# Optimization experiments

Hardware: AMD Instinct MI355X
Metric: run time of the kernel (lower is better)

The kernel has to match this reference:

```python
import jax, jax.numpy as jnp
import numpy as np

N_FILTERS = 100
WINDOWS = (2, 3, 4, 5)
B, S, W, D = 64, 400, 16, 64
VOCAB, HID = 96, 128


def setup_inputs() -> dict:
    key = jax.random.key(0)
    ks = jax.random.split(key, 16)
    inp = {
        'char_idxs': jax.random.randint(ks[0], (B, S, W), 0, VOCAB),
        'char_vectors': jax.random.normal(ks[1], (VOCAB, D), jnp.float32),
        'filt2': jax.random.normal(ks[2], (N_FILTERS, 2 * D), jnp.float32) * 0.05,
        'filt3': jax.random.normal(ks[3], (N_FILTERS, 3 * D), jnp.float32) * 0.05,
        'filt4': jax.random.normal(ks[4], (N_FILTERS, 4 * D), jnp.float32) * 0.05,
        'filt5': jax.random.normal(ks[5], (N_FILTERS, 5 * D), jnp.float32) * 0.05,
        'w_proj': jax.random.normal(ks[6], (HID, 4 * N_FILTERS), jnp.float32) * 0.05,
        't_w0': jax.random.normal(ks[7], (HID, HID), jnp.float32) * 0.05,
        't_b0': jax.random.normal(ks[8], (HID,), jnp.float32) * 0.05,
        't_w1': jax.random.normal(ks[9], (HID, HID), jnp.float32) * 0.05,
        't_b1': jax.random.normal(ks[10], (HID,), jnp.float32) * 0.05,
        'g_w0': jax.random.normal(ks[11], (HID, HID), jnp.float32) * 0.05,
        'g_b0': jax.random.normal(ks[12], (HID,), jnp.float32) * 0.05,
        'g_w1': jax.random.normal(ks[13], (HID, HID), jnp.float32) * 0.05,
        'g_b1': jax.random.normal(ks[14], (HID,), jnp.float32) * 0.05,
    }
    return inp


def _conv_branch(embed, filt, w):
    # embed: [B, S, W, D]; filt: [100, w*D]
    b, s, wl, d = embed.shape
    L = wl - w + 1  # valid positions
    idx = jnp.arange(L)[:, None] + jnp.arange(w)  # [L, w]
    xw = embed[:, :, idx, :].reshape(b, s, L, w * d)  # [B,S,L,w*D]
    h = jnp.tanh(jnp.einsum('bslk,fk->bslf', xw, filt))  # [B,S,L,100]
    return h.max(axis=2)  # max-pool over all positions -> [B,S,100]


def reference(char_idxs, char_vectors, filt2, filt3, filt4, filt5, w_proj,
              t_w0, t_b0, t_w1, t_b1, g_w0, g_b0, g_w1, g_b1):
    embed = char_vectors[char_idxs]  # [B,S,W,D]
    outs = jnp.concatenate(
        [_conv_branch(embed, f, w) for f, w in zip((filt2, filt3, filt4, filt5), WINDOWS)],
        axis=-1)  # [B,S,400]
    x = outs @ w_proj.T  # no-bias linear -> [B,S,HID]
    # 2-layer highway: x = g*relu(Wt x + bt) + (1-g)*x, g = sigmoid(Wg x + bg)
    for tw, tb, gw, gb in ((t_w0, t_b0, g_w0, g_b0), (t_w1, t_b1, g_w1, g_b1)):
        g = jax.nn.sigmoid(x @ gw.T + gb)
        t = jax.nn.relu(x @ tw.T + tb)
        x = g * t + (1.0 - g) * x
    return x
```

## Files before the change

### kernel.cpp

```cpp
#include <hip/hip_runtime.h>

#define NT     25600
#define WCH    16
#define DIM    64
#define VOCAB  96
#define HID    128
#define FPAD   104
#define NSLOT  14
#define TROW   (NSLOT * FPAD)
#define KP     416
#define TOKB   16
#define CLP    424
#define XLP    136

typedef __attribute__((ext_vector_type(8))) _Float16 h8;
typedef __attribute__((ext_vector_type(4))) float f32x4;

__device__ __forceinline__ h8 hmax8(h8 a, h8 b) {
  h8 r;
#pragma unroll
  for (int i = 0; i < 8; ++i) r[i] = a[i] > b[i] ? a[i] : b[i];
  return r;
}

__device__ __forceinline__ float tanh_fast(float m) {
  m = fminf(fmaxf(m, -15.f), 15.f);
  float e = __expf(2.f * m);
  return (e - 1.f) / (e + 1.f);
}

__global__ __launch_bounds__(256) void k_prep(
    const float* __restrict__ cv,
    const float* __restrict__ f2, const float* __restrict__ f3,
    const float* __restrict__ f4, const float* __restrict__ f5,
    const float* __restrict__ wproj,
    const float* __restrict__ tw0, const float* __restrict__ gw0,
    const float* __restrict__ tw1, const float* __restrict__ gw1,
    _Float16* __restrict__ T, _Float16* __restrict__ wprojP,
    _Float16* __restrict__ hw) {
  __shared__ float fS[100 * 65];
  __shared__ float cvS[32 * 65];
  const int tid = threadIdx.x;
  const int b = blockIdx.x;

  if (b < 42) {
    const int slot = b / 3, cg = b % 3;
    int wi, j;
    if (slot < 2)      { wi = 0; j = slot; }
    else if (slot < 5) { wi = 1; j = slot - 2; }
    else if (slot < 9) { wi = 2; j = slot - 5; }
    else               { wi = 3; j = slot - 9; }
    const float* filt = (wi == 0) ? f2 : (wi == 1) ? f3 : (wi == 2) ? f4 : f5;
    const int rowlen = (wi + 2) * DIM;
    for (int idx = tid; idx < 100 * DIM; idx += 256) {
      int f = idx >> 6, d = idx & 63;
      fS[f * 65 + d] = filt[f * rowlen + j * DIM + d];
    }
    for (int idx = tid; idx < 32 * DIM; idx += 256) {
      int c = idx >> 6, d = idx & 63;
      cvS[c * 65 + d] = cv[(cg * 32 + c) * DIM + d];
    }
    __syncthreads();
    for (int o = tid; o < 32 * FPAD; o += 256) {
      int cl = o & 31, fo = o >> 5;
      float s = 0.f;
      if (fo < 100) {
#pragma unroll 8
        for (int d = 0; d < DIM; ++d) s += cvS[cl * 65 + d] * fS[fo * 65 + d];
      }
      T[(size_t)(cg * 32 + cl) * TROW + slot * FPAD + fo] = (_Float16)s;
    }
  } else if (b < 106) {
    const int bb = b - 42;
    const int n = bb * 2 + (tid >> 7);
    const int k0 = tid & 127;
    for (int k = k0; k < KP; k += 128) {
      int wi = (k < 104) ? 0 : (k < 208) ? 1 : (k < 312) ? 2 : 3;
      int f = k - wi * FPAD;
      wprojP[n * KP + k] =
          (f < 100) ? (_Float16)wproj[n * 400 + wi * 100 + f] : (_Float16)0.f;
    }
  } else {
    const int idx = (b - 106) * 256 + tid;
    const int which = idx >> 14, r = idx & 16383;
    const float* src = (which == 0) ? tw0 : (which == 1) ? gw0
                     : (which == 2) ? tw1 : gw1;
    hw[idx] = (_Float16)src[r];
  }
}

template<int WI>
__device__ __forceinline__ void conv_win(const _Float16* __restrict__ T,
                                         const int* __restrict__ chS,
                                         _Float16* __restrict__ convL, int tid) {
  if (tid >= TOKB * 13) return;
  constexpr int W = WI + 2, L = 15 - WI;
  constexpr int SB = (WI == 0) ? 0 : (WI == 1) ? 2 : (WI == 2) ? 5 : 9;
  const int token = (tid * 1262) >> 14;
  const int octet = tid - token * 13;
  const int* chp = chS + token * WCH;
  const _Float16* Tb = T + SB * FPAD + octet * 8;
  h8 m;
  {
    h8 s = *(const h8*)(Tb + chp[0]);
#pragma unroll
    for (int j = 1; j < W; ++j) s += *(const h8*)(Tb + chp[j] + j * FPAD);
    m = s;
  }
#pragma unroll
  for (int l = 1; l < L; ++l) {
    h8 s = *(const h8*)(Tb + chp[l]);
#pragma unroll
    for (int j = 1; j < W; ++j) s += *(const h8*)(Tb + chp[l + j] + j * FPAD);
    m = hmax8(m, s);
  }
  h8 r;
#pragma unroll
  for (int i = 0; i < 8; ++i) r[i] = (_Float16)tanh_fast((float)m[i]);
  *(h8*)(convL + token * CLP + WI * FPAD + octet * 8) = r;
}

__global__ __launch_bounds__(256) void k_fused(
    const int* __restrict__ chars,
    const _Float16* __restrict__ T,
    const _Float16* __restrict__ wprojP,
    const _Float16* __restrict__ hw,
    const float* __restrict__ tb0, const float* __restrict__ tb1,
    const float* __restrict__ gb0, const float* __restrict__ gb1,
    float* __restrict__ out) {
  __shared__ __align__(16) _Float16 convL[TOKB * CLP];
  __shared__ __align__(16) _Float16 xbf[TOKB * XLP];
  __shared__ __align__(16) int chS[TOKB * WCH];

  const int tid = threadIdx.x;
  const int wave = tid >> 6, lane = tid & 63;
  const int m16 = lane & 15, quad = lane >> 4;
  const int tok0 = blockIdx.x * TOKB;
  const f32x4 zero = {0.f, 0.f, 0.f, 0.f};

  chS[tid] = chars[tok0 * WCH + tid] * TROW;
  __syncthreads();

  conv_win<0>(T, chS, convL, tid);
  conv_win<1>(T, chS, convL, tid);
  conv_win<2>(T, chS, convL, tid);
  conv_win<3>(T, chS, convL, tid);
  __syncthreads();

  const int hcA = wave * 16 + m16;
  const int hcB = hcA + 64;
  f32x4 xpA = zero, xpB = zero;
  for (int kstep = 0; kstep < 13; ++kstep) {
    const int ko = kstep * 32 + quad * 8;
    h8 a  = *(const h8*)(convL + m16 * CLP + ko);
    h8 b0 = *(const h8*)(wprojP + (size_t)hcA * KP + ko);
    h8 b1 = *(const h8*)(wprojP + (size_t)hcB * KP + ko);
    xpA = __builtin_amdgcn_mfma_f32_16x16x32_f16(a, b0, xpA, 0, 0, 0);
    xpB = __builtin_amdgcn_mfma_f32_16x16x32_f16(a, b1, xpB, 0, 0, 0);
  }

#pragma unroll
  for (int r = 0; r < 4; ++r) {
    xbf[(quad * 4 + r) * XLP + hcA]      = (_Float16)xpA[r];
    xbf[(quad * 4 + r) * XLP + 64 + hcA] = (_Float16)xpB[r];
  }
  __syncthreads();

#pragma unroll
  for (int layer = 0; layer < 2; ++layer) {
    const _Float16* tw = hw + (layer ? 2 : 0) * HID * HID;
    const _Float16* gw = hw + (layer ? 3 : 1) * HID * HID;
    const float* tbv = layer ? tb1 : tb0;
    const float* gbv = layer ? gb1 : gb0;
    float btA = tbv[hcA], bgA = gbv[hcA];
    float btB = tbv[hcB], bgB = gbv[hcB];

    f32x4 atA = zero, atB = zero, agA = zero, agB = zero;
#pragma unroll
    for (int kstep = 0; kstep < 4; ++kstep) {
      const int ko = kstep * 32 + quad * 8;
      h8 a   = *(const h8*)(xbf + m16 * XLP + ko);
      h8 bt0 = *(const h8*)(tw + (size_t)hcA * HID + ko);
      h8 bt1 = *(const h8*)(tw + (size_t)hcB * HID + ko);
      h8 bg0 = *(const h8*)(gw + (size_t)hcA * HID + ko);
      h8 bg1 = *(const h8*)(gw + (size_t)hcB * HID + ko);
      atA = __builtin_amdgcn_mfma_f32_16x16x32_f16(a, bt0, atA, 0, 0, 0);
      atB = __builtin_amdgcn_mfma_f32_16x16x32_f16(a, bt1, atB, 0, 0, 0);
      agA = __builtin_amdgcn_mfma_f32_16x16x32_f16(a, bg0, agA, 0, 0, 0);
      agB = __builtin_amdgcn_mfma_f32_16x16x32_f16(a, bg1, agB, 0, 0, 0);
    }
    __syncthreads();

#pragma unroll
    for (int r = 0; r < 4; ++r) {
      float gA = 1.f / (1.f + __expf(-(agA[r] + bgA)));
      float gB = 1.f / (1.f + __expf(-(agB[r] + bgB)));
      float tA = fmaxf(atA[r] + btA, 0.f);
      float tB = fmaxf(atB[r] + btB, 0.f);
      float xA = gA * tA + (1.f - gA) * xpA[r];
      float xB = gB * tB + (1.f - gB) * xpB[r];
      xpA[r] = xA; xpB[r] = xB;
      int row = quad * 4 + r;
      if (layer == 0) {
        xbf[row * XLP + hcA]      = (_Float16)xA;
        xbf[row * XLP + 64 + hcA] = (_Float16)xB;
      } else {
        out[(size_t)(tok0 + row) * HID + hcA]      = xA;
        out[(size_t)(tok0 + row) * HID + 64 + hcA] = xB;
      }
    }
    if (layer == 0) __syncthreads();
  }
}

extern "C" void kernel_launch(void* const* d_in, const int* in_sizes, int n_in,
                              void* d_out, int out_size, void* d_ws, size_t ws_size,
                              hipStream_t stream) {
  (void)in_sizes; (void)n_in; (void)out_size; (void)ws_size;
  const int* chars = (const int*)d_in[0];
  const float* cv  = (const float*)d_in[1];
  const float* f2  = (const float*)d_in[2];
  const float* f3  = (const float*)d_in[3];
  const float* f4  = (const float*)d_in[4];
  const float* f5  = (const float*)d_in[5];
  const float* wpj = (const float*)d_in[6];
  const float* tw0 = (const float*)d_in[7];
  const float* tb0 = (const float*)d_in[8];
  const float* tw1 = (const float*)d_in[9];
  const float* tb1 = (const float*)d_in[10];
  const float* gw0 = (const float*)d_in[11];
  const float* gb0 = (const float*)d_in[12];
  const float* gw1 = (const float*)d_in[13];
  const float* gb1 = (const float*)d_in[14];
  float* out = (float*)d_out;

  char* ws = (char*)d_ws;
  _Float16* T      = (_Float16*)ws;
  _Float16* wprojP = (_Float16*)(ws + 279552);
  _Float16* hw     = (_Float16*)(ws + 279552 + 106496);

  k_prep<<<362, 256, 0, stream>>>(cv, f2, f3, f4, f5, wpj, tw0, gw0, tw1, gw1,
                                  T, wprojP, hw);
  k_fused<<<NT / TOKB, 256, 0, stream>>>(chars, T, wprojP, hw,
                                         tb0, tb1, gb0, gb1, out);
}
```

Measured before the change: 182.5 us.

## Swizzle LDS conv layout, rebalance conv work per thread, cheaper tanh/sigmoid

Pads the filter-projection table slots to a 128-element pitch. The LDS conv and highway activation buffers move to a slot-major XOR-swizzled layout so the MFMA A-operand reads avoid bank conflicts. Conv work is split into 416 items over two rounds, each pairing window sizes (2+5, 3+4) to balance load, with character offsets held in registers. tanh and sigmoid switch to the exp2 and rcp builtins, and launch bounds request 8 blocks per CU. A leftover dead sigmoid expression is computed and then overwritten; it may be eliminated by the compiler.

```diff
diff --git a/kernel.cpp b/kernel.cpp
--- a/kernel.cpp
+++ b/kernel.cpp
@@ -6,27 +6,19 @@
 #define VOCAB  96
 #define HID    128
 #define FPAD   104
+#define SPITCH 128
 #define NSLOT  14
-#define TROW   (NSLOT * FPAD)
+#define TROW   (NSLOT * SPITCH)
 #define KP     416
 #define TOKB   16
-#define CLP    424
-#define XLP    136
 
 typedef __attribute__((ext_vector_type(8))) _Float16 h8;
 typedef __attribute__((ext_vector_type(4))) float f32x4;
 
-__device__ __forceinline__ h8 hmax8(h8 a, h8 b) {
-  h8 r;
-#pragma unroll
-  for (int i = 0; i < 8; ++i) r[i] = a[i] > b[i] ? a[i] : b[i];
-  return r;
-}
-
 __device__ __forceinline__ float tanh_fast(float m) {
-  m = fminf(fmaxf(m, -15.f), 15.f);
-  float e = __expf(2.f * m);
-  return (e - 1.f) / (e + 1.f);
+  float t = fminf(fmaxf(m, -9.f), 9.f);
+  float e = __builtin_amdgcn_exp2f(t * 2.885390082f);
+  return 1.f - 2.f * __builtin_amdgcn_rcpf(e + 1.f);
 }
 
 __global__ __launch_bounds__(256) void k_prep(
@@ -68,7 +60,7 @@
 #pragma unroll 8
         for (int d = 0; d < DIM; ++d) s += cvS[cl * 65 + d] * fS[fo * 65 + d];
       }
-      T[(size_t)(cg * 32 + cl) * TROW + slot * FPAD + fo] = (_Float16)s;
+      T[(size_t)(cg * 32 + cl) * TROW + slot * SPITCH + fo] = (_Float16)s;
     }
   } else if (b < 106) {
     const int bb = b - 42;
@@ -89,38 +81,35 @@
   }
 }
 
+template<int W>
+__device__ __forceinline__ h8 rowsum(const _Float16* __restrict__ Tb,
+                                     const int* __restrict__ ch, int l) {
+  h8 s = *(const h8*)(Tb + ch[l]);
+#pragma unroll
+  for (int j = 1; j < W; ++j) s += *(const h8*)(Tb + ch[l + j] + j * SPITCH);
+  return s;
+}
+
 template<int WI>
-__device__ __forceinline__ void conv_win(const _Float16* __restrict__ T,
-                                         const int* __restrict__ chS,
-                                         _Float16* __restrict__ convL, int tid) {
-  if (tid >= TOKB * 13) return;
+__device__ __forceinline__ void conv_store(const _Float16* __restrict__ T,
+                                           const int* __restrict__ ch,
+                                           _Float16* __restrict__ convA,
+                                           int token, int octet) {
   constexpr int W = WI + 2, L = 15 - WI;
   constexpr int SB = (WI == 0) ? 0 : (WI == 1) ? 2 : (WI == 2) ? 5 : 9;
-  const int token = (tid * 1262) >> 14;
-  const int octet = tid - token * 13;
-  const int* chp = chS + token * WCH;
-  const _Float16* Tb = T + SB * FPAD + octet * 8;
-  h8 m;
-  {
-    h8 s = *(const h8*)(Tb + chp[0]);
-#pragma unroll
-    for (int j = 1; j < W; ++j) s += *(const h8*)(Tb + chp[j] + j * FPAD);
-    m = s;
-  }
-#pragma unroll
-  for (int l = 1; l < L; ++l) {
-    h8 s = *(const h8*)(Tb + chp[l]);
-#pragma unroll
-    for (int j = 1; j < W; ++j) s += *(const h8*)(Tb + chp[l + j] + j * FPAD);
-    m = hmax8(m, s);
-  }
+  const _Float16* Tb = T + SB * SPITCH + octet * 8;
+  h8 m = rowsum<W>(Tb, ch, 0);
+#pragma unroll
+  for (int l = 1; l < L; ++l)
+    m = __builtin_elementwise_max(m, rowsum<W>(Tb, ch, l));
   h8 r;
 #pragma unroll
   for (int i = 0; i < 8; ++i) r[i] = (_Float16)tanh_fast((float)m[i]);
-  *(h8*)(convL + token * CLP + WI * FPAD + octet * 8) = r;
-}
-
-__global__ __launch_bounds__(256) void k_fused(
+  const int slot8 = WI * 13 + octet;
+  *(h8*)(convA + slot8 * 128 + ((token ^ (slot8 & 15)) * 8)) = r;
+}
+
+__global__ __launch_bounds__(256, 8) void k_fused(
     const int* __restrict__ chars,
     const _Float16* __restrict__ T,
     const _Float16* __restrict__ wprojP,
@@ -128,8 +117,8 @@
     const float* __restrict__ tb0, const float* __restrict__ tb1,
     const float* __restrict__ gb0, const float* __restrict__ gb1,
     float* __restrict__ out) {
-  __shared__ __align__(16) _Float16 convL[TOKB * CLP];
-  __shared__ __align__(16) _Float16 xbf[TOKB * XLP];
+  __shared__ __align__(16) _Float16 convA[52 * 128];
+  __shared__ __align__(16) _Float16 xA[16 * 128];
   __shared__ __align__(16) int chS[TOKB * WCH];
 
   const int tid = threadIdx.x;
@@ -141,28 +130,45 @@
   chS[tid] = chars[tok0 * WCH + tid] * TROW;
   __syncthreads();
 
-  conv_win<0>(T, chS, convL, tid);
-  conv_win<1>(T, chS, convL, tid);
-  conv_win<2>(T, chS, convL, tid);
-  conv_win<3>(T, chS, convL, tid);
+#pragma unroll
+  for (int rnd = 0; rnd < 2; ++rnd) {
+    const int p = tid + rnd * 256;
+    if (p < 416) {
+      const int token = p / 26;
+      const int sub = p - token * 26;
+      const int half = sub >= 13;
+      const int octet = half ? sub - 13 : sub;
+      int ch[WCH];
+#pragma unroll
+      for (int i = 0; i < WCH; ++i) ch[i] = chS[token * WCH + i];
+      if (half == 0) {
+        conv_store<0>(T, ch, convA, token, octet);
+        conv_store<3>(T, ch, convA, token, octet);
+      } else {
+        conv_store<1>(T, ch, convA, token, octet);
+        conv_store<2>(T, ch, convA, token, octet);
+      }
+    }
+  }
   __syncthreads();
 
   const int hcA = wave * 16 + m16;
   const int hcB = hcA + 64;
   f32x4 xpA = zero, xpB = zero;
-  for (int kstep = 0; kstep < 13; ++kstep) {
-    const int ko = kstep * 32 + quad * 8;
-    h8 a  = *(const h8*)(convL + m16 * CLP + ko);
-    h8 b0 = *(const h8*)(wprojP + (size_t)hcA * KP + ko);
-    h8 b1 = *(const h8*)(wprojP + (size_t)hcB * KP + ko);
+  for (int ks = 0; ks < 13; ++ks) {
+    const int slot8 = ks * 4 + quad;
+    h8 a  = *(const h8*)(convA + slot8 * 128 + ((m16 ^ (slot8 & 15)) * 8));
+    h8 b0 = *(const h8*)(wprojP + (size_t)hcA * KP + ks * 32 + quad * 8);
+    h8 b1 = *(const h8*)(wprojP + (size_t)hcB * KP + ks * 32 + quad * 8);
     xpA = __builtin_amdgcn_mfma_f32_16x16x32_f16(a, b0, xpA, 0, 0, 0);
     xpB = __builtin_amdgcn_mfma_f32_16x16x32_f16(a, b1, xpB, 0, 0, 0);
   }
 
 #pragma unroll
   for (int r = 0; r < 4; ++r) {
-    xbf[(quad * 4 + r) * XLP + hcA]      = (_Float16)xpA[r];
-    xbf[(quad * 4 + r) * XLP + 64 + hcA] = (_Float16)xpB[r];
+    int row = quad * 4 + r;
+    xA[(hcA >> 3) * 128 + row * 8 + (hcA & 7)]        = (_Float16)xpA[r];
+    xA[((hcA + 64) >> 3) * 128 + row * 8 + (hcA & 7)] = (_Float16)xpB[r];
   }
   __syncthreads();
 
@@ -177,9 +183,9 @@
 
     f32x4 atA = zero, atB = zero, agA = zero, agB = zero;
 #pragma unroll
-    for (int kstep = 0; kstep < 4; ++kstep) {
-      const int ko = kstep * 32 + quad * 8;
-      h8 a   = *(const h8*)(xbf + m16 * XLP + ko);
+    for (int ks = 0; ks < 4; ++ks) {
+      const int ko = ks * 32 + quad * 8;
+      h8 a   = *(const h8*)(xA + (ks * 4 + quad) * 128 + m16 * 8);
       h8 bt0 = *(const h8*)(tw + (size_t)hcA * HID + ko);
       h8 bt1 = *(const h8*)(tw + (size_t)hcB * HID + ko);
       h8 bg0 = *(const h8*)(gw + (size_t)hcA * HID + ko);
@@ -193,20 +199,23 @@
 
 #pragma unroll
     for (int r = 0; r < 4; ++r) {
-      float gA = 1.f / (1.f + __expf(-(agA[r] + bgA)));
-      float gB = 1.f / (1.f + __expf(-(agB[r] + bgB)));
+      float gA = 1.f - __builtin_amdgcn_rcpf(1.f + __builtin_amdgcn_exp2f(
+                     (agA[r] + bgA) * 1.442695041f) * 0.f + 1.f +
+                     __builtin_amdgcn_exp2f(-(agA[r] + bgA) * 1.442695041f) - 1.f);
+      gA = 1.f / (1.f + __builtin_amdgcn_exp2f(-(agA[r] + bgA) * 1.442695041f));
+      float gB = 1.f / (1.f + __builtin_amdgcn_exp2f(-(agB[r] + bgB) * 1.442695041f));
       float tA = fmaxf(atA[r] + btA, 0.f);
       float tB = fmaxf(atB[r] + btB, 0.f);
-      float xA = gA * tA + (1.f - gA) * xpA[r];
-      float xB = gB * tB + (1.f - gB) * xpB[r];
-      xpA[r] = xA; xpB[r] = xB;
+      float xAv = gA * tA + (1.f - gA) * xpA[r];
+      float xBv = gB * tB + (1.f - gB) * xpB[r];
+      xpA[r] = xAv; xpB[r] = xBv;
       int row = quad * 4 + r;
       if (layer == 0) {
-        xbf[row * XLP + hcA]      = (_Float16)xA;
-        xbf[row * XLP + 64 + hcA] = (_Float16)xB;
+        xA[(hcA >> 3) * 128 + row * 8 + (hcA & 7)]        = (_Float16)xAv;
+        xA[((hcA + 64) >> 3) * 128 + row * 8 + (hcA & 7)] = (_Float16)xBv;
       } else {
-        out[(size_t)(tok0 + row) * HID + hcA]      = xA;
-        out[(size_t)(tok0 + row) * HID + 64 + hcA] = xB;
+        out[(size_t)(tok0 + row) * HID + hcA]      = xAv;
+        out[(size_t)(tok0 + row) * HID + 64 + hcA] = xBv;
       }
     }
     if (layer == 0) __syncthreads();
@@ -236,8 +245,8 @@
 
   char* ws = (char*)d_ws;
   _Float16* T      = (_Float16*)ws;
-  _Float16* wprojP = (_Float16*)(ws + 279552);
-  _Float16* hw     = (_Float16*)(ws + 279552 + 106496);
+  _Float16* wprojP = (_Float16*)(ws + 344064);
+  _Float16* hw     = (_Float16*)(ws + 344064 + 106496);
 
   k_prep<<<362, 256, 0, stream>>>(cv, f2, f3, f4, f5, wpj, tw0, gw0, tw1, gw1,
                                   T, wprojP, hw);
```

Measured after the change: 202.1 us. 1.11x slower.

## Stage octet-major conv tables in LDS and quadruple tokens per block

Applied to the files above, without the earlier changes.

The fused kernel now processes 64 tokens per block instead of 16. The precomputed char-filter table is reorganised octet-major so each 21 KB slice can be staged into LDS, which turns random global gathers into LDS gathers. The projection and highway MFMAs now reuse each loaded weight fragment across four M-tiles, and the A operand uses a swizzled LDS layout. It also switches tanh and sigmoid to exp2/rcp intrinsics. The cost is 13 barrier-separated staging rounds, about 77 KB of LDS per block (lower occupancy), and a quarter as many blocks.

```diff
diff --git a/kernel.cpp b/kernel.cpp
--- a/kernel.cpp
+++ b/kernel.cpp
@@ -5,28 +5,16 @@
 #define DIM    64
 #define VOCAB  96
 #define HID    128
-#define FPAD   104
-#define NSLOT  14
-#define TROW   (NSLOT * FPAD)
 #define KP     416
-#define TOKB   16
-#define CLP    424
-#define XLP    136
+#define TOKB   64
 
 typedef __attribute__((ext_vector_type(8))) _Float16 h8;
 typedef __attribute__((ext_vector_type(4))) float f32x4;
 
-__device__ __forceinline__ h8 hmax8(h8 a, h8 b) {
-  h8 r;
-#pragma unroll
-  for (int i = 0; i < 8; ++i) r[i] = a[i] > b[i] ? a[i] : b[i];
-  return r;
-}
-
 __device__ __forceinline__ float tanh_fast(float m) {
-  m = fminf(fmaxf(m, -15.f), 15.f);
-  float e = __expf(2.f * m);
-  return (e - 1.f) / (e + 1.f);
+  float t = fminf(fmaxf(m, -9.f), 9.f);
+  float e = __builtin_amdgcn_exp2f(t * 2.885390082f);
+  return 1.f - 2.f * __builtin_amdgcn_rcpf(e + 1.f);
 }
 
 __global__ __launch_bounds__(256) void k_prep(
@@ -36,15 +24,15 @@
     const float* __restrict__ wproj,
     const float* __restrict__ tw0, const float* __restrict__ gw0,
     const float* __restrict__ tw1, const float* __restrict__ gw1,
-    _Float16* __restrict__ T, _Float16* __restrict__ wprojP,
+    _Float16* __restrict__ T2, _Float16* __restrict__ wprojP,
     _Float16* __restrict__ hw) {
   __shared__ float fS[100 * 65];
-  __shared__ float cvS[32 * 65];
+  __shared__ float cvS[8 * 65];
   const int tid = threadIdx.x;
   const int b = blockIdx.x;
 
-  if (b < 42) {
-    const int slot = b / 3, cg = b % 3;
+  if (b < 168) {
+    const int slot = b / 12, cg = b - slot * 12;
     int wi, j;
     if (slot < 2)      { wi = 0; j = slot; }
     else if (slot < 5) { wi = 1; j = slot - 2; }
@@ -56,32 +44,32 @@
       int f = idx >> 6, d = idx & 63;
       fS[f * 65 + d] = filt[f * rowlen + j * DIM + d];
     }
-    for (int idx = tid; idx < 32 * DIM; idx += 256) {
+    for (int idx = tid; idx < 8 * DIM; idx += 256) {
       int c = idx >> 6, d = idx & 63;
-      cvS[c * 65 + d] = cv[(cg * 32 + c) * DIM + d];
+      cvS[c * 65 + d] = cv[(cg * 8 + c) * DIM + d];
     }
     __syncthreads();
-    for (int o = tid; o < 32 * FPAD; o += 256) {
-      int cl = o & 31, fo = o >> 5;
+    for (int idx = tid; idx < 8 * 104; idx += 256) {
+      int cl = idx / 104, f = idx - cl * 104;
       float s = 0.f;
-      if (fo < 100) {
+      if (f < 100) {
 #pragma unroll 8
-        for (int d = 0; d < DIM; ++d) s += cvS[cl * 65 + d] * fS[fo * 65 + d];
+        for (int d = 0; d < DIM; ++d) s += cvS[cl * 65 + d] * fS[f * 65 + d];
       }
-      T[(size_t)(cg * 32 + cl) * TROW + slot * FPAD + fo] = (_Float16)s;
-    }
-  } else if (b < 106) {
-    const int bb = b - 42;
-    const int n = bb * 2 + (tid >> 7);
-    const int k0 = tid & 127;
-    for (int k = k0; k < KP; k += 128) {
-      int wi = (k < 104) ? 0 : (k < 208) ? 1 : (k < 312) ? 2 : 3;
-      int f = k - wi * FPAD;
+      T2[((size_t)(f >> 3) * 14 + slot) * 768 + (cg * 8 + cl) * 8 + (f & 7)] =
+          (_Float16)s;
+    }
+  } else if (b < 232) {
+    const int n = (b - 168) * 2 + (tid >> 7);
+    for (int k = tid & 127; k < KP; k += 128) {
+      int s8 = k >> 3;
+      int wi = s8 / 13;
+      int fl = (s8 - wi * 13) * 8 + (k & 7);
       wprojP[n * KP + k] =
-          (f < 100) ? (_Float16)wproj[n * 400 + wi * 100 + f] : (_Float16)0.f;
+          (fl < 100) ? (_Float16)wproj[n * 400 + wi * 100 + fl] : (_Float16)0.f;
     }
   } else {
-    const int idx = (b - 106) * 256 + tid;
+    const int idx = (b - 232) * 256 + tid;
     const int which = idx >> 14, r = idx & 16383;
     const float* src = (which == 0) ? tw0 : (which == 1) ? gw0
                      : (which == 2) ? tw1 : gw1;
@@ -90,47 +78,46 @@
 }
 
 template<int WI>
-__device__ __forceinline__ void conv_win(const _Float16* __restrict__ T,
-                                         const int* __restrict__ chS,
-                                         _Float16* __restrict__ convL, int tid) {
-  if (tid >= TOKB * 13) return;
+__device__ __forceinline__ void conv_oct(const _Float16* __restrict__ Ts,
+                                         const int* __restrict__ ch,
+                                         _Float16* __restrict__ convA,
+                                         int token, int o) {
   constexpr int W = WI + 2, L = 15 - WI;
   constexpr int SB = (WI == 0) ? 0 : (WI == 1) ? 2 : (WI == 2) ? 5 : 9;
-  const int token = (tid * 1262) >> 14;
-  const int octet = tid - token * 13;
-  const int* chp = chS + token * WCH;
-  const _Float16* Tb = T + SB * FPAD + octet * 8;
   h8 m;
   {
-    h8 s = *(const h8*)(Tb + chp[0]);
-#pragma unroll
-    for (int j = 1; j < W; ++j) s += *(const h8*)(Tb + chp[j] + j * FPAD);
+    h8 s = *(const h8*)(Ts + SB * 768 + ch[0]);
+#pragma unroll
+    for (int j = 1; j < W; ++j) s += *(const h8*)(Ts + (SB + j) * 768 + ch[j]);
     m = s;
   }
 #pragma unroll
   for (int l = 1; l < L; ++l) {
-    h8 s = *(const h8*)(Tb + chp[l]);
-#pragma unroll
-    for (int j = 1; j < W; ++j) s += *(const h8*)(Tb + chp[l + j] + j * FPAD);
-    m = hmax8(m, s);
+    h8 s = *(const h8*)(Ts + SB * 768 + ch[l]);
+#pragma unroll
+    for (int j = 1; j < W; ++j) s += *(const h8*)(Ts + (SB + j) * 768 + ch[l + j]);
+    m = __builtin_elementwise_max(m, s);
   }
   h8 r;
 #pragma unroll
   for (int i = 0; i < 8; ++i) r[i] = (_Float16)tanh_fast((float)m[i]);
-  *(h8*)(convL + token * CLP + WI * FPAD + octet * 8) = r;
+  const int s8 = WI * 13 + o;
+  *(h8*)(convA + (s8 * 64 + (token & 48) + ((token & 15) ^ (s8 & 15))) * 8) = r;
 }
 
 __global__ __launch_bounds__(256) void k_fused(
     const int* __restrict__ chars,
-    const _Float16* __restrict__ T,
+    const _Float16* __restrict__ T2,
     const _Float16* __restrict__ wprojP,
     const _Float16* __restrict__ hw,
     const float* __restrict__ tb0, const float* __restrict__ tb1,
     const float* __restrict__ gb0, const float* __restrict__ gb1,
     float* __restrict__ out) {
-  __shared__ __align__(16) _Float16 convL[TOKB * CLP];
-  __shared__ __align__(16) _Float16 xbf[TOKB * XLP];
-  __shared__ __align__(16) int chS[TOKB * WCH];
+  __shared__ __align__(16) char lds[78848];
+  _Float16* Ts    = (_Float16*)lds;
+  _Float16* xA    = (_Float16*)lds;
+  _Float16* convA = (_Float16*)(lds + 21504);
+  int*      chS   = (int*)(lds + 21504 + 53248);
 
   const int tid = threadIdx.x;
   const int wave = tid >> 6, lane = tid & 63;
@@ -138,32 +125,62 @@
   const int tok0 = blockIdx.x * TOKB;
   const f32x4 zero = {0.f, 0.f, 0.f, 0.f};
 
-  chS[tid] = chars[tok0 * WCH + tid] * TROW;
+#pragma unroll
+  for (int k = 0; k < 4; ++k) {
+    int idx = tid + k * 256;
+    int t = idx >> 4, i = idx & 15;
+    chS[i * 64 + t] = chars[(tok0 + t) * WCH + i] * 8;
+  }
   __syncthreads();
 
-  conv_win<0>(T, chS, convL, tid);
-  conv_win<1>(T, chS, convL, tid);
-  conv_win<2>(T, chS, convL, tid);
-  conv_win<3>(T, chS, convL, tid);
+  const int token = tid & 63;
+  int ch[WCH];
+#pragma unroll
+  for (int i = 0; i < WCH; ++i) ch[i] = chS[i * 64 + token];
+
+  for (int o = 0; o < 13; ++o) {
+    if (o) __syncthreads();
+    const _Float16* src = T2 + (size_t)o * 10752;
+    for (int r = tid; r < 1344; r += 256)
+      *(h8*)(Ts + r * 8) = *(const h8*)(src + r * 8);
+    __syncthreads();
+    switch ((wave + o) & 3) {
+      case 0: conv_oct<0>(Ts, ch, convA, token, o); break;
+      case 1: conv_oct<1>(Ts, ch, convA, token, o); break;
+      case 2: conv_oct<2>(Ts, ch, convA, token, o); break;
+      default: conv_oct<3>(Ts, ch, convA, token, o); break;
+    }
+  }
   __syncthreads();
 
   const int hcA = wave * 16 + m16;
   const int hcB = hcA + 64;
-  f32x4 xpA = zero, xpB = zero;
-  for (int kstep = 0; kstep < 13; ++kstep) {
-    const int ko = kstep * 32 + quad * 8;
-    h8 a  = *(const h8*)(convL + m16 * CLP + ko);
-    h8 b0 = *(const h8*)(wprojP + (size_t)hcA * KP + ko);
-    h8 b1 = *(const h8*)(wprojP + (size_t)hcB * KP + ko);
-    xpA = __builtin_amdgcn_mfma_f32_16x16x32_f16(a, b0, xpA, 0, 0, 0);
-    xpB = __builtin_amdgcn_mfma_f32_16x16x32_f16(a, b1, xpB, 0, 0, 0);
-  }
-
-#pragma unroll
-  for (int r = 0; r < 4; ++r) {
-    xbf[(quad * 4 + r) * XLP + hcA]      = (_Float16)xpA[r];
-    xbf[(quad * 4 + r) * XLP + 64 + hcA] = (_Float16)xpB[r];
-  }
+  f32x4 xp[4][2];
+#pragma unroll
+  for (int mt = 0; mt < 4; ++mt) { xp[mt][0] = zero; xp[mt][1] = zero; }
+
+  for (int ks = 0; ks < 13; ++ks) {
+    const int s8 = ks * 4 + quad;
+    h8 b0 = *(const h8*)(wprojP + (size_t)hcA * KP + s8 * 8);
+    h8 b1 = *(const h8*)(wprojP + (size_t)hcB * KP + s8 * 8);
+#pragma unroll
+    for (int mt = 0; mt < 4; ++mt) {
+      h8 a = *(const h8*)(convA + (s8 * 64 + mt * 16 + (m16 ^ (s8 & 15))) * 8);
+      xp[mt][0] = __builtin_amdgcn_mfma_f32_16x16x32_f16(a, b0, xp[mt][0], 0, 0, 0);
+      xp[mt][1] = __builtin_amdgcn_mfma_f32_16x16x32_f16(a, b1, xp[mt][1], 0, 0, 0);
+    }
+  }
+
+#pragma unroll
+  for (int mt = 0; mt < 4; ++mt)
+#pragma unroll
+    for (int nt = 0; nt < 2; ++nt) {
+      int col = nt * 64 + hcA;
+#pragma unroll
+      for (int r = 0; r < 4; ++r)
+        xA[(col >> 3) * 512 + (mt * 16 + quad * 4 + r) * 8 + (col & 7)] =
+            (_Float16)xp[mt][nt][r];
+    }
   __syncthreads();
 
 #pragma unroll
@@ -175,40 +192,50 @@
     float btA = tbv[hcA], bgA = gbv[hcA];
     float btB = tbv[hcB], bgB = gbv[hcB];
 
-    f32x4 atA = zero, atB = zero, agA = zero, agB = zero;
-#pragma unroll
-    for (int kstep = 0; kstep < 4; ++kstep) {
-      const int ko = kstep * 32 + quad * 8;
-      h8 a   = *(const h8*)(xbf + m16 * XLP + ko);
+    f32x4 at[4][2], ag[4][2];
+#pragma unroll
+    for (int mt = 0; mt < 4; ++mt) {
+      at[mt][0] = zero; at[mt][1] = zero;
+      ag[mt][0] = zero; ag[mt][1] = zero;
+    }
+#pragma unroll
+    for (int ks = 0; ks < 4; ++ks) {
+      const int ko = ks * 32 + quad * 8;
       h8 bt0 = *(const h8*)(tw + (size_t)hcA * HID + ko);
       h8 bt1 = *(const h8*)(tw + (size_t)hcB * HID + ko);
       h8 bg0 = *(const h8*)(gw + (size_t)hcA * HID + ko);
       h8 bg1 = *(const h8*)(gw + (size_t)hcB * HID + ko);
-      atA = __builtin_amdgcn_mfma_f32_16x16x32_f16(a, bt0, atA, 0, 0, 0);
-      atB = __builtin_amdgcn_mfma_f32_16x16x32_f16(a, bt1, atB, 0, 0, 0);
-      agA = __builtin_amdgcn_mfma_f32_16x16x32_f16(a, bg0, agA, 0, 0, 0);
-      agB = __builtin_amdgcn_mfma_f32_16x16x32_f16(a, bg1, agB, 0, 0, 0);
+#pragma unroll
+      for (int mt = 0; mt < 4; ++mt) {
+        h8 a = *(const h8*)(xA + (ks * 4 + quad) * 512 + (mt * 16 + m16) * 8);
+        at[mt][0] = __builtin_amdgcn_mfma_f32_16x16x32_f16(a, bt0, at[mt][0], 0, 0, 0);
+        at[mt][1] = __builtin_amdgcn_mfma_f32_16x16x32_f16(a, bt1, at[mt][1], 0, 0, 0);
+        ag[mt][0] = __builtin_amdgcn_mfma_f32_16x16x32_f16(a, bg0, ag[mt][0], 0, 0, 0);
+        ag[mt][1] = __builtin_amdgcn_mfma_f32_16x16x32_f16(a, bg1, ag[mt][1], 0, 0, 0);
+      }
     }
     __syncthreads();
 
 #pragma unroll
-    for (int r = 0; r < 4; ++r) {
-      float gA = 1.f / (1.f + __expf(-(agA[r] + bgA)));
-      float gB = 1.f / (1.f + __expf(-(agB[r] + bgB)));
-      float tA = fmaxf(atA[r] + btA, 0.f);
-      float tB = fmaxf(atB[r] + btB, 0.f);
-      float xA = gA * tA + (1.f - gA) * xpA[r];
-      float xB = gB * tB + (1.f - gB) * xpB[r];
-      xpA[r] = xA; xpB[r] = xB;
-      int row = quad * 4 + r;
-      if (layer == 0) {
-        xbf[row * XLP + hcA]      = (_Float16)xA;
-        xbf[row * XLP + 64 + hcA] = (_Float16)xB;
-      } else {
-        out[(size_t)(tok0 + row) * HID + hcA]      = xA;
-        out[(size_t)(tok0 + row) * HID + 64 + hcA] = xB;
+    for (int mt = 0; mt < 4; ++mt)
+#pragma unroll
+      for (int nt = 0; nt < 2; ++nt) {
+        float bt = nt ? btB : btA, bg = nt ? bgB : bgA;
+        int col = nt * 64 + hcA;
+#pragma unroll
+        for (int r = 0; r < 4; ++r) {
+          float g = 1.f / (1.f + __builtin_amdgcn_exp2f(
+                               -(ag[mt][nt][r] + bg) * 1.442695041f));
+          float tt = fmaxf(at[mt][nt][r] + bt, 0.f);
+          float xn = g * tt + (1.f - g) * xp[mt][nt][r];
+          xp[mt][nt][r] = xn;
+          int row = mt * 16 + quad * 4 + r;
+          if (layer == 0)
+            xA[(col >> 3) * 512 + row * 8 + (col & 7)] = (_Float16)xn;
+          else
+            out[(size_t)(tok0 + row) * HID + col] = xn;
+        }
       }
-    }
     if (layer == 0) __syncthreads();
   }
 }
@@ -235,12 +262,12 @@
   float* out = (float*)d_out;
 
   char* ws = (char*)d_ws;
-  _Float16* T      = (_Float16*)ws;
+  _Float16* T2     = (_Float16*)ws;
   _Float16* wprojP = (_Float16*)(ws + 279552);
   _Float16* hw     = (_Float16*)(ws + 279552 + 106496);
 
-  k_prep<<<362, 256, 0, stream>>>(cv, f2, f3, f4, f5, wpj, tw0, gw0, tw1, gw1,
-                                  T, wprojP, hw);
-  k_fused<<<NT / TOKB, 256, 0, stream>>>(chars, T, wprojP, hw,
+  k_prep<<<488, 256, 0, stream>>>(cv, f2, f3, f4, f5, wpj, tw0, gw0, tw1, gw1,
+                                  T2, wprojP, hw);
+  k_fused<<<NT / TOKB, 256, 0, stream>>>(chars, T2, wprojP, hw,
                                          tb0, tb1, gb0, gb1, out);
 }
```

Result: faster. 175.4 us (-3.9%).
